# Kernel tuning notes

Measured on AMD Instinct MI355X. Metric: run time of the kernel, lower is better.

## Reference

```python
import jax, jax.numpy as jnp
import numpy as np


def _gcn_conv(x, edge_index, W, b):
    """PyG-style GCNConv: linear, add self-loops, symmetric norm, scatter-add, bias."""
    n = x.shape[0]
    h = x @ W  # [N, F_out]
    loops = jnp.arange(n, dtype=edge_index.dtype)
    row = jnp.concatenate([edge_index[0], loops])  # source
    col = jnp.concatenate([edge_index[1], loops])  # target
    deg = jax.ops.segment_sum(jnp.ones_like(col, dtype=h.dtype), col, num_segments=n)
    dinv = jnp.where(deg > 0, jax.lax.rsqrt(deg), 0.0)
    norm = dinv[row] * dinv[col]  # [E+N]
    msg = h[row] * norm[:, None]  # edge-wise gather + scale
    out = jax.ops.segment_sum(msg, col, num_segments=n)  # scatter-add
    return out + b


def setup_inputs() -> dict:
    key = jax.random.key(0)
    k1, k2, k3, k4 = jax.random.split(key, 4)
    N, E, F_in, F_out = 50000, 800000, 128, 64
    hidden = 2 * F_out
    x = jax.random.normal(k1, (N, F_in), dtype=jnp.float32)
    edge_index = jax.random.randint(k2, (2, E), 0, N, dtype=jnp.int64)
    # Glorot-ish init for weights
    W1 = jax.random.normal(k3, (F_in, hidden), dtype=jnp.float32) / np.sqrt(F_in)
    b1 = jnp.zeros((hidden,), dtype=jnp.float32)
    W2 = jax.random.normal(k4, (hidden, F_out), dtype=jnp.float32) / np.sqrt(hidden)
    b2 = jnp.zeros((F_out,), dtype=jnp.float32)
    return {"x": x, "edge_index": edge_index, "W1": W1, "b1": b1, "W2": W2, "b2": b2}


def reference(x, edge_index, W1, b1, W2, b2):
    h = _gcn_conv(x, edge_index, W1, b1)
    h = jax.nn.relu(h)
    out = _gcn_conv(h, edge_index, W2, b2)
    return out
```

## Files before the change

### kernel.cpp

```cpp
#include <hip/hip_runtime.h>
#include <stdint.h>


typedef _Float16 h2v   __attribute__((ext_vector_type(2)));
typedef _Float16 h4v   __attribute__((ext_vector_type(4)));
typedef _Float16 f16x8 __attribute__((ext_vector_type(8)));
typedef float    f32x4 __attribute__((ext_vector_type(4)));

__global__ void k_prep(const float* __restrict__ W1, const float* __restrict__ W2,
                       _Float16* __restrict__ WT1, _Float16* __restrict__ WT2,
                       uint32_t* __restrict__ bcnt) {
    int i = blockIdx.x * blockDim.x + threadIdx.x;
    if (i < 256) bcnt[i] = 0u;
    if (i < 128 * 128) {
        int f = i >> 7, k = i & 127;
        WT1[i] = (_Float16)W1[k * 128 + f];
    }
    int j = i - 128 * 128;
    if (j >= 0 && j < 64 * 128) {
        int f = j >> 7, k = j & 127;
        WT2[j] = (_Float16)W2[k * 64 + f];
    }
}

__global__ __launch_bounds__(256)
void k_bhist(const int* __restrict__ col, uint32_t* __restrict__ bcnt, int E) {
    __shared__ uint32_t h[256];
    const int t = threadIdx.x;
    h[t] = 0u; __syncthreads();
    const int base = blockIdx.x * 4096;
#pragma unroll
    for (int k = 0; k < 16; ++k) {
        int i = base + k * 256 + t;
        if (i < E) atomicAdd(&h[__builtin_nontemporal_load(&col[i]) >> 8], 1u);
    }
    __syncthreads();
    if (h[t]) atomicAdd(&bcnt[t], h[t]);
}

__global__ void k_bscan(const uint32_t* __restrict__ bcnt, uint32_t* __restrict__ boff,
                        uint32_t* __restrict__ bfill, uint32_t* __restrict__ rp,
                        int NB, int n) {
    __shared__ uint32_t s[256];
    const int t = threadIdx.x;
    uint32_t v = (t < NB) ? bcnt[t] : 0u;
    s[t] = v; __syncthreads();
    for (int off = 1; off < 256; off <<= 1) {
        uint32_t u = (t >= off) ? s[t - off] : 0u;
        __syncthreads();
        s[t] += u;
        __syncthreads();
    }
    uint32_t ex = s[t] - v;
    if (t < NB) { boff[t] = ex; bfill[t] = ex; }
    if (t == NB - 1) { boff[NB] = s[t]; rp[n] = s[t]; }
}

__global__ __launch_bounds__(256)
void k_bin(const int* __restrict__ row, const int* __restrict__ col,
           uint32_t* __restrict__ bfill, uint32_t* __restrict__ ebuf, int E) {
    __shared__ uint32_t hcnt[256], hbase[256];
    const int t = threadIdx.x;
    hcnt[t] = 0u; __syncthreads();
    const int base = blockIdx.x * 4096;
#pragma unroll
    for (int k = 0; k < 16; ++k) {
        int i = base + k * 256 + t;
        if (i < E) atomicAdd(&hcnt[__builtin_nontemporal_load(&col[i]) >> 8], 1u);
    }
    __syncthreads();
    hbase[t] = atomicAdd(&bfill[t], hcnt[t]);
    hcnt[t] = 0u;
    __syncthreads();
#pragma unroll
    for (int k = 0; k < 16; ++k) {
        int i = base + k * 256 + t;
        if (i < E) {
            int c = __builtin_nontemporal_load(&col[i]);
            int r = __builtin_nontemporal_load(&row[i]);
            int b = c >> 8;
            uint32_t slot = hbase[b] + atomicAdd(&hcnt[b], 1u);
            ebuf[slot] = (uint32_t)r | ((uint32_t)(c & 255) << 16);
        }
    }
}

__global__ __launch_bounds__(256)
void k_bucket(const uint32_t* __restrict__ boff, const uint32_t* __restrict__ ebuf,
              uint32_t* __restrict__ rp, float* __restrict__ dinv,
              uint16_t* __restrict__ esrc, int n) {
    __shared__ uint32_t lcnt[256], lbase[256];
    const int t = threadIdx.x;
    const int b = blockIdx.x;
    const int base_c = b << 8;
    const int nc = min(256, n - base_c);
    const uint32_t start = boff[b], end = boff[b + 1];

    lcnt[t] = 0u; __syncthreads();
    for (uint32_t i = start + t; i < end; i += 256)
        atomicAdd(&lcnt[ebuf[i] >> 16], 1u);
    __syncthreads();

    const uint32_t v = lcnt[t];
    lbase[t] = v; __syncthreads();
    for (int off = 1; off < 256; off <<= 1) {
        uint32_t u = (t >= off) ? lbase[t - off] : 0u;
        __syncthreads();
        lbase[t] += u;
        __syncthreads();
    }
    const uint32_t ex = lbase[t] - v;
    if (t < nc) {
        rp[base_c + t]   = start + ex;
        dinv[base_c + t] = rsqrtf((float)(v + 1u));
    }
    lbase[t] = start + ex;
    lcnt[t]  = 0u;
    __syncthreads();

    for (uint32_t i = start + t; i < end; i += 256) {
        uint32_t vv = ebuf[i];
        uint32_t cl = vv >> 16;
        uint32_t slot = lbase[cl] + atomicAdd(&lcnt[cl], 1u);
        esrc[slot] = (uint16_t)(vv & 0xffffu);
    }
}

template <int FOUT, typename XT>
__global__ __launch_bounds__(256)
void k_gemm_mfma(const XT* __restrict__ X, const _Float16* __restrict__ WT,
                 const float* __restrict__ dinv, _Float16* __restrict__ H, int n) {
    constexpr int K  = 128;
    constexpr int KP = K + 8;
    constexpr int NT = FOUT / 16;
    __shared__ _Float16 Wl[FOUT * KP];

    const int tid = threadIdx.x;
    for (int i = tid; i < FOUT * (K / 8); i += 256) {
        int f = i / (K / 8), kc = i % (K / 8);
        *reinterpret_cast<f16x8*>(&Wl[f * KP + kc * 8]) =
            *reinterpret_cast<const f16x8*>(&WT[f * K + kc * 8]);
    }
    __syncthreads();

    const int wid  = tid >> 6;
    const int lane = tid & 63;
    const int col  = lane & 15;
    const int krow = lane >> 4;
    const int node = blockIdx.x * 64 + wid * 16 + col;
    const int nld  = node < n ? node : n - 1;

    f32x4 acc[NT];
#pragma unroll
    for (int t = 0; t < NT; ++t) acc[t] = (f32x4){0.f, 0.f, 0.f, 0.f};

#pragma unroll
    for (int ks = 0; ks < 4; ++ks) {
        const int k0 = ks * 32 + krow * 8;
        f16x8 b;
        if constexpr (sizeof(XT) == 4) {
            float4 x0 = *reinterpret_cast<const float4*>(&X[(size_t)nld * K + k0]);
            float4 x1 = *reinterpret_cast<const float4*>(&X[(size_t)nld * K + k0 + 4]);
            b[0] = (_Float16)x0.x; b[1] = (_Float16)x0.y;
            b[2] = (_Float16)x0.z; b[3] = (_Float16)x0.w;
            b[4] = (_Float16)x1.x; b[5] = (_Float16)x1.y;
            b[6] = (_Float16)x1.z; b[7] = (_Float16)x1.w;
        } else {
            b = *reinterpret_cast<const f16x8*>(&X[(size_t)nld * K + k0]);
        }
#pragma unroll
        for (int t = 0; t < NT; ++t) {
            f16x8 a = *reinterpret_cast<const f16x8*>(&Wl[(t * 16 + col) * KP + k0]);
            acc[t] = __builtin_amdgcn_mfma_f32_16x16x32_f16(a, b, acc[t], 0, 0, 0);
        }
    }

    if (node < n) {
        const float dv = dinv[node];
#pragma unroll
        for (int t = 0; t < NT; ++t) {
            h4v hv;
            hv.x = (_Float16)(acc[t][0] * dv);
            hv.y = (_Float16)(acc[t][1] * dv);
            hv.z = (_Float16)(acc[t][2] * dv);
            hv.w = (_Float16)(acc[t][3] * dv);
            *reinterpret_cast<h4v*>(&H[(size_t)node * FOUT + t * 16 + krow * 4]) = hv;
        }
    }
}

__global__ void k_agg128(const _Float16* __restrict__ H, const uint32_t* __restrict__ rp,
                         const uint16_t* __restrict__ es, const float* __restrict__ dinv,
                         const float* __restrict__ bias, _Float16* __restrict__ out, int n) {
    int wave = (blockIdx.x * blockDim.x + threadIdx.x) >> 6;
    int lane = threadIdx.x & 63;
    if (wave >= n) return;
    const int v = wave;
    int p = (int)rp[v];
    const int e = (int)rp[v + 1];
    const int c0 = lane * 2;

    float ax = 0.f, ay = 0.f;
    for (; p + 8 <= e; p += 8) {
        int ss[8];
#pragma unroll
        for (int u = 0; u < 8; ++u) ss[u] = (int)__builtin_nontemporal_load(&es[p + u]);
        h2v hh[8];
#pragma unroll
        for (int u = 0; u < 8; ++u)
            hh[u] = *reinterpret_cast<const h2v*>(&H[(size_t)ss[u] * 128 + c0]);
#pragma unroll
        for (int u = 0; u < 8; ++u) { ax += (float)hh[u].x; ay += (float)hh[u].y; }
    }
    if (p + 4 <= e) {
        int ss[4];
#pragma unroll
        for (int u = 0; u < 4; ++u) ss[u] = (int)__builtin_nontemporal_load(&es[p + u]);
        h2v hh[4];
#pragma unroll
        for (int u = 0; u < 4; ++u)
            hh[u] = *reinterpret_cast<const h2v*>(&H[(size_t)ss[u] * 128 + c0]);
#pragma unroll
        for (int u = 0; u < 4; ++u) { ax += (float)hh[u].x; ay += (float)hh[u].y; }
        p += 4;
    }
    for (; p < e; ++p) {
        int s = (int)__builtin_nontemporal_load(&es[p]);
        h2v h0 = *reinterpret_cast<const h2v*>(&H[(size_t)s * 128 + c0]);
        ax += (float)h0.x; ay += (float)h0.y;
    }
    h2v sv = *reinterpret_cast<const h2v*>(&H[(size_t)v * 128 + c0]);
    ax += (float)sv.x; ay += (float)sv.y;
    const float dv = dinv[v];
    ax = fmaxf(fmaf(dv, ax, bias[c0]), 0.f);
    ay = fmaxf(fmaf(dv, ay, bias[c0 + 1]), 0.f);
    h2v o; o.x = (_Float16)ax; o.y = (_Float16)ay;
    *reinterpret_cast<h2v*>(&out[(size_t)v * 128 + c0]) = o;
}

__global__ void k_agg64(const _Float16* __restrict__ H, const uint32_t* __restrict__ rp,
                        const uint16_t* __restrict__ es, const float* __restrict__ dinv,
                        const float* __restrict__ bias, float* __restrict__ out, int n) {
    int wave = (blockIdx.x * blockDim.x + threadIdx.x) >> 6;
    int lane = threadIdx.x & 63;
    if (wave >= n) return;
    const int v = wave;
    const int half = lane >> 5;
    const int c0 = (lane & 31) * 2;
    int p = (int)rp[v] + half;
    const int e = (int)rp[v + 1];

    float ax = 0.f, ay = 0.f;
    for (; p + 6 < e; p += 8) {
        int ss[4];
#pragma unroll
        for (int u = 0; u < 4; ++u) ss[u] = (int)__builtin_nontemporal_load(&es[p + 2 * u]);
        h2v hh[4];
#pragma unroll
        for (int u = 0; u < 4; ++u)
            hh[u] = *reinterpret_cast<const h2v*>(&H[(size_t)ss[u] * 64 + c0]);
#pragma unroll
        for (int u = 0; u < 4; ++u) { ax += (float)hh[u].x; ay += (float)hh[u].y; }
    }
    for (; p < e; p += 2) {
        int s = (int)__builtin_nontemporal_load(&es[p]);
        h2v h0 = *reinterpret_cast<const h2v*>(&H[(size_t)s * 64 + c0]);
        ax += (float)h0.x; ay += (float)h0.y;
    }
    ax += __shfl_xor(ax, 32);
    ay += __shfl_xor(ay, 32);
    if (lane < 32) {
        h2v sv = *reinterpret_cast<const h2v*>(&H[(size_t)v * 64 + c0]);
        ax += (float)sv.x; ay += (float)sv.y;
        const float dv = dinv[v];
        ax = fmaf(dv, ax, bias[c0]);
        ay = fmaf(dv, ay, bias[c0 + 1]);
        *reinterpret_cast<float2*>(&out[(size_t)v * 64 + c0]) = make_float2(ax, ay);
    }
}

extern "C" void kernel_launch(void* const* d_in, const int* in_sizes, int n_in,
                              void* d_out, int out_size, void* d_ws, size_t ws_size,
                              hipStream_t stream) {
    const float* x  = (const float*)d_in[0];
    const int*   ei = (const int*)d_in[1];
    const float* W1 = (const float*)d_in[2];
    const float* b1 = (const float*)d_in[3];
    const float* W2 = (const float*)d_in[4];
    const float* b2 = (const float*)d_in[5];
    float* out = (float*)d_out;

    const int hidden = in_sizes[3];
    const int fin    = in_sizes[2] / hidden;
    const int n      = in_sizes[0] / fin;
    const int E      = in_sizes[1] / 2;
    const int* rowi = ei;
    const int* coli = ei + E;
    (void)n_in; (void)out_size; (void)ws_size;

    char* ws = (char*)d_ws;
    size_t off = 0;
    auto alloc = [&](size_t bytes) -> void* {
        off = (off + 255) & ~(size_t)255;
        void* p = ws + off;
        off += bytes;
        return p;
    };
    uint32_t*  bcnt = (uint32_t*) alloc(256 * 4);
    uint32_t*  boff = (uint32_t*) alloc(257 * 4);
    uint32_t*  bfill= (uint32_t*) alloc(256 * 4);
    uint32_t*  rp   = (uint32_t*) alloc((size_t)(n + 1) * 4);
    float*     dinv = (float*)    alloc((size_t)n * 4);
    uint32_t*  ebuf = (uint32_t*) alloc((size_t)E * 4);
    uint16_t*  esrc = (uint16_t*) alloc((size_t)E * 2);
    _Float16*  h1   = (_Float16*) alloc((size_t)n * 128 * 2);
    _Float16*  g1   = (_Float16*) alloc((size_t)n * 128 * 2);
    _Float16*  WT1  = (_Float16*) alloc(128 * 128 * 2);
    _Float16*  WT2  = (_Float16*) alloc(64 * 128 * 2);
    _Float16*  h2   = h1;

    const int nb256 = (n + 255) / 256;
    const int NB    = (n + 255) >> 8;
    const int NW    = (E + 4095) >> 12;

    k_prep  <<<nb256, 256, 0, stream>>>(W1, W2, WT1, WT2, bcnt);
    k_bhist <<<NW, 256, 0, stream>>>(coli, bcnt, E);
    k_bscan <<<1, 256, 0, stream>>>(bcnt, boff, bfill, rp, NB, n);
    k_bin   <<<NW, 256, 0, stream>>>(rowi, coli, bfill, ebuf, E);
    k_bucket<<<NB, 256, 0, stream>>>(boff, ebuf, rp, dinv, esrc, n);

    const int gb = (n + 63) / 64;
    k_gemm_mfma<128, float>   <<<gb, 256, 0, stream>>>(x, WT1, dinv, h1, n);
    k_agg128<<<(n + 3) / 4, 256, 0, stream>>>(h1, rp, esrc, dinv, b1, g1, n);
    k_gemm_mfma<64, _Float16> <<<gb, 256, 0, stream>>>(g1, WT2, dinv, h2, n);
    k_agg64 <<<(n + 3) / 4, 256, 0, stream>>>(h2, rp, esrc, dinv, b2, out, n);
}
```

Baseline: 210.0 us.

## Fuse second GEMM into first aggregation and pad edge lists to 8

```diff
diff --git a/kernel.cpp b/kernel.cpp
--- a/kernel.cpp
+++ b/kernel.cpp
@@ -8,18 +8,23 @@
 typedef float    f32x4 __attribute__((ext_vector_type(4)));
 
 __global__ void k_prep(const float* __restrict__ W1, const float* __restrict__ W2,
-                       _Float16* __restrict__ WT1, _Float16* __restrict__ WT2,
-                       uint32_t* __restrict__ bcnt) {
+                       _Float16* __restrict__ WT1, h2v* __restrict__ W2P,
+                       uint32_t* __restrict__ bcnt,
+                       _Float16* __restrict__ h1, _Float16* __restrict__ h2, int n) {
     int i = blockIdx.x * blockDim.x + threadIdx.x;
     if (i < 256) bcnt[i] = 0u;
+    if (i < 128) h1[(size_t)n * 128 + i] = (_Float16)0.f;
+    if (i < 64)  h2[(size_t)n * 64  + i] = (_Float16)0.f;
     if (i < 128 * 128) {
         int f = i >> 7, k = i & 127;
         WT1[i] = (_Float16)W1[k * 128 + f];
     }
-    int j = i - 128 * 128;
-    if (j >= 0 && j < 64 * 128) {
-        int f = j >> 7, k = j & 127;
-        WT2[j] = (_Float16)W2[k * 64 + f];
+    if (i < 4096) {
+        int k2 = i >> 6, f = i & 63;
+        h2v pr;
+        pr.x = (_Float16)W2[(2 * k2) * 64 + f];
+        pr.y = (_Float16)W2[(2 * k2 + 1) * 64 + f];
+        W2P[i] = pr;
     }
 }
 
@@ -39,8 +44,7 @@
 }
 
 __global__ void k_bscan(const uint32_t* __restrict__ bcnt, uint32_t* __restrict__ boff,
-                        uint32_t* __restrict__ bfill, uint32_t* __restrict__ rp,
-                        int NB, int n) {
+                        uint32_t* __restrict__ bfill, int NB) {
     __shared__ uint32_t s[256];
     const int t = threadIdx.x;
     uint32_t v = (t < NB) ? bcnt[t] : 0u;
@@ -53,7 +57,7 @@
     }
     uint32_t ex = s[t] - v;
     if (t < NB) { boff[t] = ex; bfill[t] = ex; }
-    if (t == NB - 1) { boff[NB] = s[t]; rp[n] = s[t]; }
+    if (t == NB - 1) boff[NB] = s[t];
 }
 
 __global__ __launch_bounds__(256)
@@ -87,41 +91,49 @@
 
 __global__ __launch_bounds__(256)
 void k_bucket(const uint32_t* __restrict__ boff, const uint32_t* __restrict__ ebuf,
-              uint32_t* __restrict__ rp, float* __restrict__ dinv,
-              uint16_t* __restrict__ esrc, int n) {
-    __shared__ uint32_t lcnt[256], lbase[256];
+              uint32_t* __restrict__ rps, uint32_t* __restrict__ rpe,
+              float* __restrict__ dinv, uint16_t* __restrict__ esrc, int n) {
+    __shared__ uint32_t lcnt[256], lscan[256], lbase[256], lfill[256];
+    __shared__ uint32_t s_total;
     const int t = threadIdx.x;
     const int b = blockIdx.x;
     const int base_c = b << 8;
     const int nc = min(256, n - base_c);
     const uint32_t start = boff[b], end = boff[b + 1];
+    const uint32_t pstart = (start + (uint32_t)b * 2048u + 7u) & ~7u;
 
     lcnt[t] = 0u; __syncthreads();
     for (uint32_t i = start + t; i < end; i += 256)
         atomicAdd(&lcnt[ebuf[i] >> 16], 1u);
     __syncthreads();
 
-    const uint32_t v = lcnt[t];
-    lbase[t] = v; __syncthreads();
+    const uint32_t v  = lcnt[t];
+    const uint32_t pc = (v + 7u) & ~7u;
+    lscan[t] = pc; __syncthreads();
     for (int off = 1; off < 256; off <<= 1) {
-        uint32_t u = (t >= off) ? lbase[t - off] : 0u;
+        uint32_t u = (t >= off) ? lscan[t - off] : 0u;
         __syncthreads();
-        lbase[t] += u;
+        lscan[t] += u;
         __syncthreads();
     }
-    const uint32_t ex = lbase[t] - v;
+    const uint32_t pex = lscan[t] - pc;
+    if (t == 255) s_total = lscan[255];
     if (t < nc) {
-        rp[base_c + t]   = start + ex;
+        rps[base_c + t]  = pstart + pex;
+        rpe[base_c + t]  = pstart + pex + pc;
         dinv[base_c + t] = rsqrtf((float)(v + 1u));
     }
-    lbase[t] = start + ex;
-    lcnt[t]  = 0u;
-    __syncthreads();
-
+    lbase[t] = pstart + pex;
+    lfill[t] = 0u;
+    __syncthreads();
+    const uint32_t total = s_total;
+    for (uint32_t i = t; i < total; i += 256)
+        esrc[pstart + i] = (uint16_t)n;
+    __syncthreads();
     for (uint32_t i = start + t; i < end; i += 256) {
         uint32_t vv = ebuf[i];
         uint32_t cl = vv >> 16;
-        uint32_t slot = lbase[cl] + atomicAdd(&lcnt[cl], 1u);
+        uint32_t slot = lbase[cl] + atomicAdd(&lfill[cl], 1u);
         esrc[slot] = (uint16_t)(vv & 0xffffu);
     }
 }
@@ -189,83 +201,93 @@
     }
 }
 
-__global__ void k_agg128(const _Float16* __restrict__ H, const uint32_t* __restrict__ rp,
-                         const uint16_t* __restrict__ es, const float* __restrict__ dinv,
-                         const float* __restrict__ bias, _Float16* __restrict__ out, int n) {
-    int wave = (blockIdx.x * blockDim.x + threadIdx.x) >> 6;
-    int lane = threadIdx.x & 63;
-    if (wave >= n) return;
-    const int v = wave;
-    int p = (int)rp[v];
-    const int e = (int)rp[v + 1];
+__global__ __launch_bounds__(256)
+void k_aggmm(const _Float16* __restrict__ H, const uint32_t* __restrict__ rps,
+             const uint32_t* __restrict__ rpe, const uint16_t* __restrict__ es,
+             const float* __restrict__ dinv, const float* __restrict__ b1,
+             const h2v* __restrict__ W2P, _Float16* __restrict__ h2out, int n) {
+    __shared__ h2v   W2l[64 * 64];
+    __shared__ float2 g1row[4][64];
+    const int tid = threadIdx.x;
+    for (int i = tid; i < 1024; i += 256)
+        reinterpret_cast<uint4*>(W2l)[i] = reinterpret_cast<const uint4*>(W2P)[i];
+    __syncthreads();
+
+    const int wid = tid >> 6, lane = tid & 63;
+    const int v = blockIdx.x * 4 + wid;
+    if (v >= n) return;
     const int c0 = lane * 2;
+    int p = (int)rps[v];
+    const int e = (int)rpe[v];
 
     float ax = 0.f, ay = 0.f;
-    for (; p + 8 <= e; p += 8) {
-        int ss[8];
-#pragma unroll
-        for (int u = 0; u < 8; ++u) ss[u] = (int)__builtin_nontemporal_load(&es[p + u]);
+    for (; p + 16 <= e; p += 16) {
+        uint4 wa = *reinterpret_cast<const uint4*>(&es[p]);
+        uint4 wb = *reinterpret_cast<const uint4*>(&es[p + 8]);
+        uint32_t id[16] = { wa.x & 0xffffu, wa.x >> 16, wa.y & 0xffffu, wa.y >> 16,
+                            wa.z & 0xffffu, wa.z >> 16, wa.w & 0xffffu, wa.w >> 16,
+                            wb.x & 0xffffu, wb.x >> 16, wb.y & 0xffffu, wb.y >> 16,
+                            wb.z & 0xffffu, wb.z >> 16, wb.w & 0xffffu, wb.w >> 16 };
+        h2v hh[16];
+#pragma unroll
+        for (int u = 0; u < 16; ++u)
+            hh[u] = *reinterpret_cast<const h2v*>(&H[(size_t)id[u] * 128 + c0]);
+#pragma unroll
+        for (int u = 0; u < 16; ++u) { ax += (float)hh[u].x; ay += (float)hh[u].y; }
+    }
+    if (p < e) {
+        uint4 wa = *reinterpret_cast<const uint4*>(&es[p]);
+        uint32_t id[8] = { wa.x & 0xffffu, wa.x >> 16, wa.y & 0xffffu, wa.y >> 16,
+                           wa.z & 0xffffu, wa.z >> 16, wa.w & 0xffffu, wa.w >> 16 };
         h2v hh[8];
 #pragma unroll
         for (int u = 0; u < 8; ++u)
-            hh[u] = *reinterpret_cast<const h2v*>(&H[(size_t)ss[u] * 128 + c0]);
+            hh[u] = *reinterpret_cast<const h2v*>(&H[(size_t)id[u] * 128 + c0]);
 #pragma unroll
         for (int u = 0; u < 8; ++u) { ax += (float)hh[u].x; ay += (float)hh[u].y; }
-    }
-    if (p + 4 <= e) {
-        int ss[4];
-#pragma unroll
-        for (int u = 0; u < 4; ++u) ss[u] = (int)__builtin_nontemporal_load(&es[p + u]);
-        h2v hh[4];
-#pragma unroll
-        for (int u = 0; u < 4; ++u)
-            hh[u] = *reinterpret_cast<const h2v*>(&H[(size_t)ss[u] * 128 + c0]);
-#pragma unroll
-        for (int u = 0; u < 4; ++u) { ax += (float)hh[u].x; ay += (float)hh[u].y; }
-        p += 4;
-    }
-    for (; p < e; ++p) {
-        int s = (int)__builtin_nontemporal_load(&es[p]);
-        h2v h0 = *reinterpret_cast<const h2v*>(&H[(size_t)s * 128 + c0]);
-        ax += (float)h0.x; ay += (float)h0.y;
     }
     h2v sv = *reinterpret_cast<const h2v*>(&H[(size_t)v * 128 + c0]);
     ax += (float)sv.x; ay += (float)sv.y;
     const float dv = dinv[v];
-    ax = fmaxf(fmaf(dv, ax, bias[c0]), 0.f);
-    ay = fmaxf(fmaf(dv, ay, bias[c0 + 1]), 0.f);
-    h2v o; o.x = (_Float16)ax; o.y = (_Float16)ay;
-    *reinterpret_cast<h2v*>(&out[(size_t)v * 128 + c0]) = o;
-}
-
-__global__ void k_agg64(const _Float16* __restrict__ H, const uint32_t* __restrict__ rp,
-                        const uint16_t* __restrict__ es, const float* __restrict__ dinv,
-                        const float* __restrict__ bias, float* __restrict__ out, int n) {
+    float gx = fmaxf(fmaf(dv, ax, b1[c0]), 0.f);
+    float gy = fmaxf(fmaf(dv, ay, b1[c0 + 1]), 0.f);
+    g1row[wid][lane] = make_float2(gx, gy);
+
+    float acc = 0.f;
+#pragma unroll 8
+    for (int k2 = 0; k2 < 64; ++k2) {
+        float2 g = g1row[wid][k2];
+        h2v w = W2l[k2 * 64 + lane];
+        acc += g.x * (float)w.x + g.y * (float)w.y;
+    }
+    h2out[(size_t)v * 64 + lane] = (_Float16)(dv * acc);
+}
+
+__global__ __launch_bounds__(256)
+void k_agg64(const _Float16* __restrict__ H, const uint32_t* __restrict__ rps,
+             const uint32_t* __restrict__ rpe, const uint16_t* __restrict__ es,
+             const float* __restrict__ dinv, const float* __restrict__ bias,
+             float* __restrict__ out, int n) {
     int wave = (blockIdx.x * blockDim.x + threadIdx.x) >> 6;
     int lane = threadIdx.x & 63;
     if (wave >= n) return;
     const int v = wave;
     const int half = lane >> 5;
     const int c0 = (lane & 31) * 2;
-    int p = (int)rp[v] + half;
-    const int e = (int)rp[v + 1];
+    int p = (int)rps[v] + half * 8;
+    const int e = (int)rpe[v];
 
     float ax = 0.f, ay = 0.f;
-    for (; p + 6 < e; p += 8) {
-        int ss[4];
-#pragma unroll
-        for (int u = 0; u < 4; ++u) ss[u] = (int)__builtin_nontemporal_load(&es[p + 2 * u]);
-        h2v hh[4];
-#pragma unroll
-        for (int u = 0; u < 4; ++u)
-            hh[u] = *reinterpret_cast<const h2v*>(&H[(size_t)ss[u] * 64 + c0]);
-#pragma unroll
-        for (int u = 0; u < 4; ++u) { ax += (float)hh[u].x; ay += (float)hh[u].y; }
-    }
-    for (; p < e; p += 2) {
-        int s = (int)__builtin_nontemporal_load(&es[p]);
-        h2v h0 = *reinterpret_cast<const h2v*>(&H[(size_t)s * 64 + c0]);
-        ax += (float)h0.x; ay += (float)h0.y;
+    for (; p + 8 <= e; p += 16) {
+        uint4 wa = *reinterpret_cast<const uint4*>(&es[p]);
+        uint32_t id[8] = { wa.x & 0xffffu, wa.x >> 16, wa.y & 0xffffu, wa.y >> 16,
+                           wa.z & 0xffffu, wa.z >> 16, wa.w & 0xffffu, wa.w >> 16 };
+        h2v hh[8];
+#pragma unroll
+        for (int u = 0; u < 8; ++u)
+            hh[u] = *reinterpret_cast<const h2v*>(&H[(size_t)id[u] * 64 + c0]);
+#pragma unroll
+        for (int u = 0; u < 8; ++u) { ax += (float)hh[u].x; ay += (float)hh[u].y; }
     }
     ax += __shfl_xor(ax, 32);
     ay += __shfl_xor(ay, 32);
@@ -306,32 +328,30 @@
         off += bytes;
         return p;
     };
+    const int NB = (n + 255) >> 8;
     uint32_t*  bcnt = (uint32_t*) alloc(256 * 4);
     uint32_t*  boff = (uint32_t*) alloc(257 * 4);
     uint32_t*  bfill= (uint32_t*) alloc(256 * 4);
-    uint32_t*  rp   = (uint32_t*) alloc((size_t)(n + 1) * 4);
+    uint32_t*  rps  = (uint32_t*) alloc((size_t)n * 4);
+    uint32_t*  rpe  = (uint32_t*) alloc((size_t)n * 4);
     float*     dinv = (float*)    alloc((size_t)n * 4);
     uint32_t*  ebuf = (uint32_t*) alloc((size_t)E * 4);
-    uint16_t*  esrc = (uint16_t*) alloc((size_t)E * 2);
-    _Float16*  h1   = (_Float16*) alloc((size_t)n * 128 * 2);
-    _Float16*  g1   = (_Float16*) alloc((size_t)n * 128 * 2);
+    uint16_t*  esrc = (uint16_t*) alloc(((size_t)E + (size_t)NB * 2048 + 4096) * 2);
+    _Float16*  h1   = (_Float16*) alloc((size_t)(n + 1) * 128 * 2);
+    _Float16*  h2   = (_Float16*) alloc((size_t)(n + 1) * 64 * 2);
     _Float16*  WT1  = (_Float16*) alloc(128 * 128 * 2);
-    _Float16*  WT2  = (_Float16*) alloc(64 * 128 * 2);
-    _Float16*  h2   = h1;
-
-    const int nb256 = (n + 255) / 256;
-    const int NB    = (n + 255) >> 8;
-    const int NW    = (E + 4095) >> 12;
-
-    k_prep  <<<nb256, 256, 0, stream>>>(W1, W2, WT1, WT2, bcnt);
+    h2v*       W2P  = (h2v*)      alloc(64 * 64 * sizeof(h2v));
+
+    const int NW = (E + 4095) >> 12;
+
+    k_prep  <<<64, 256, 0, stream>>>(W1, W2, WT1, W2P, bcnt, h1, h2, n);
     k_bhist <<<NW, 256, 0, stream>>>(coli, bcnt, E);
-    k_bscan <<<1, 256, 0, stream>>>(bcnt, boff, bfill, rp, NB, n);
+    k_bscan <<<1, 256, 0, stream>>>(bcnt, boff, bfill, NB);
     k_bin   <<<NW, 256, 0, stream>>>(rowi, coli, bfill, ebuf, E);
-    k_bucket<<<NB, 256, 0, stream>>>(boff, ebuf, rp, dinv, esrc, n);
+    k_bucket<<<NB, 256, 0, stream>>>(boff, ebuf, rps, rpe, dinv, esrc, n);
 
     const int gb = (n + 63) / 64;
-    k_gemm_mfma<128, float>   <<<gb, 256, 0, stream>>>(x, WT1, dinv, h1, n);
-    k_agg128<<<(n + 3) / 4, 256, 0, stream>>>(h1, rp, esrc, dinv, b1, g1, n);
-    k_gemm_mfma<64, _Float16> <<<gb, 256, 0, stream>>>(g1, WT2, dinv, h2, n);
-    k_agg64 <<<(n + 3) / 4, 256, 0, stream>>>(h2, rp, esrc, dinv, b2, out, n);
-}
+    k_gemm_mfma<128, float><<<gb, 256, 0, stream>>>(x, WT1, dinv, h1, n);
+    k_aggmm <<<(n + 3) / 4, 256, 0, stream>>>(h1, rps, rpe, esrc, dinv, b1, W2P, h2, n);
+    k_agg64 <<<(n + 3) / 4, 256, 0, stream>>>(h2, rps, rpe, esrc, dinv, b2, out, n);
+}
```

Result: faster. 197.1 us (-6.2%).
